# Optimization experiments

Hardware: AMD Instinct MI355X
Metric: run time of the kernel (lower is better)

Reference implementation:

```python
import jax, jax.numpy as jnp
import numpy as np
from jax import lax

CLASSES = 6
R = 8            # zoom_factor
FEAT = 32        # DUC loops i,j in range(32)
OUT_PAD = 304    # DUC hardcodes zeros(b,6,304,304)
IMG = 256        # original image H=W -> final bilinear resize target
BN_EPS = 1e-5
DN = ('NCHW', 'OIHW', 'NCHW')


def _duc(x):
    # x: [B, classes*r*r, H', W'] ; original loop only reads top-left 32x32
    x = x[:, :, :FEAT, :FEAT]
    B = x.shape[0]
    # channel order in original: view(b, classes, r*r) -> (classes, r, r)
    y = x.reshape(B, CLASSES, R, R, FEAT, FEAT)
    y = y.transpose(0, 1, 4, 2, 5, 3).reshape(B, CLASSES, FEAT * R, FEAT * R)  # [B,6,256,256]
    pad = OUT_PAD - FEAT * R
    return jnp.pad(y, ((0, 0), (0, 0), (0, pad), (0, pad)))  # zeros ring like torch.zeros buffer


def _bilinear_align_corners(x, oh, ow):
    b, c, h, w = x.shape
    ys = jnp.linspace(0.0, h - 1.0, oh)
    xs = jnp.linspace(0.0, w - 1.0, ow)
    y0 = jnp.floor(ys).astype(jnp.int32)
    x0 = jnp.floor(xs).astype(jnp.int32)
    y1 = jnp.minimum(y0 + 1, h - 1)
    x1 = jnp.minimum(x0 + 1, w - 1)
    wy = (ys - y0)[None, None, :, None]
    wx = (xs - x0)[None, None, None, :]
    rows = x[:, :, y0, :] * (1.0 - wy) + x[:, :, y1, :] * wy          # [b,c,oh,w]
    out = rows[:, :, :, x0] * (1.0 - wx) + rows[:, :, :, x1] * wx     # [b,c,oh,ow]
    return out


def setup_inputs() -> dict:
    key = jax.random.key(0)
    ks = jax.random.split(key, 8)
    x = jax.random.normal(ks[0], (16, 5632, 32, 32), jnp.float32)
    w1 = jax.random.normal(ks[1], (512, 5632, 1, 1), jnp.float32) * 0.02
    gamma = 1.0 + 0.1 * jax.random.normal(ks[2], (512,), jnp.float32)
    beta = 0.1 * jax.random.normal(ks[3], (512,), jnp.float32)
    mean = 0.1 * jax.random.normal(ks[4], (512,), jnp.float32)
    var = jax.random.uniform(ks[5], (512,), jnp.float32, 0.5, 1.5)
    w2 = jax.random.normal(ks[6], (CLASSES * R * R, 512, 1, 1), jnp.float32) * 0.02
    b2 = jax.random.normal(ks[7], (CLASSES * R * R,), jnp.float32) * 0.02
    return {'x': x, 'w1': w1, 'gamma': gamma, 'beta': beta, 'mean': mean, 'var': var, 'w2': w2, 'b2': b2}


def reference(x, w1, gamma, beta, mean, var, w2, b2):
    # cls head: 1x1 conv with padding=1 (quirk in source) -> 34x34 map
    h = lax.conv_general_dilated(x, w1, (1, 1), ((1, 1), (1, 1)), dimension_numbers=DN)
    inv = lax.rsqrt(var + BN_EPS)
    h = (h - mean[None, :, None, None]) * (inv * gamma)[None, :, None, None] + beta[None, :, None, None]
    h = jax.nn.relu(h)  # Dropout2d is identity at inference
    h = lax.conv_general_dilated(h, w2, (1, 1), ((0, 0), (0, 0)), dimension_numbers=DN)
    h = h + b2[None, :, None, None]            # [B,384,34,34]
    h = _duc(h)                                # [B,6,304,304]
    h = jax.nn.softmax(h, axis=1)
    return _bilinear_align_corners(h, IMG, IMG)  # [B,6,256,256]
```

## Files before the change

### kernel.cpp

```cpp
#include <hip/hip_runtime.h>
#include <hip/hip_bf16.h>
#include <stdint.h>

typedef float f32x4 __attribute__((ext_vector_type(4)));
typedef short s16x8 __attribute__((ext_vector_type(8)));
typedef unsigned short u16;

__device__ __forceinline__ u16 f2bf(float f) {
  uint32_t u = __float_as_uint(f);
  u = (u + 0x7fffu + ((u >> 16) & 1u)) >> 16;
  return (u16)u;
}

__global__ void k_params(const float* __restrict__ gamma, const float* __restrict__ beta,
                         const float* __restrict__ mean, const float* __restrict__ var,
                         float* __restrict__ bnS, float* __restrict__ bnT) {
  int i = threadIdx.x;
  if (i < 512) {
    float s = gamma[i] * rsqrtf(var[i] + 1e-5f);
    bnS[i] = s;
    bnT[i] = beta[i] - mean[i] * s;
  }
}

__global__ void k_convert(const float* __restrict__ in, u16* __restrict__ out, int n4) {
  int i = blockIdx.x * blockDim.x + threadIdx.x;
  if (i < n4) {
    float4 v = ((const float4*)in)[i];
    ushort4 o;
    o.x = f2bf(v.x); o.y = f2bf(v.y); o.z = f2bf(v.z); o.w = f2bf(v.w);
    ((ushort4*)out)[i] = o;
  }
}

__global__ void k_border2(const float* __restrict__ w2, const float* __restrict__ b2,
                          const float* __restrict__ bnT, float* __restrict__ border2) {
  int o = blockIdx.x;
  int l = threadIdx.x;
  float s = 0.f;
  for (int j = 0; j < 8; ++j) {
    int c = l + 64 * j;
    s += w2[o * 512 + c] * fmaxf(bnT[c], 0.f);
  }
  for (int off = 32; off > 0; off >>= 1) s += __shfl_down(s, off, 64);
  if (l == 0) border2[o] = s + b2[o];
}

__global__ __launch_bounds__(256) void k_trans(const float* __restrict__ x, u16* __restrict__ xT,
                                               int b0, int CB) {
  int id = blockIdx.x;
  int bl = id / (88 * 16);
  int rem = id - bl * 88 * 16;
  int ktile = rem >> 4;
  int ptile = rem & 15;
  __shared__ __align__(16) u16 tile[64 * 80];
  int t = threadIdx.x;
  int kl = t >> 2;
  int pb = (t & 3) * 16;
  const float* src = x + ((size_t)(b0 + bl) * 5632 + (size_t)(ktile * 64 + kl)) * 1024
                       + ptile * 64 + pb;
#pragma unroll
  for (int j = 0; j < 4; ++j) {
    float4 v = *(const float4*)(src + j * 4);
    int p = pb + j * 4;
    tile[(p + 0) * 80 + kl] = f2bf(v.x);
    tile[(p + 1) * 80 + kl] = f2bf(v.y);
    tile[(p + 2) * 80 + kl] = f2bf(v.z);
    tile[(p + 3) * 80 + kl] = f2bf(v.w);
  }
  __syncthreads();
#pragma unroll
  for (int j = 0; j < 2; ++j) {
    int q = t + j * 256;
    int pl = q >> 3, g = q & 7;
    s16x8 v = *(const s16x8*)(tile + pl * 80 + g * 8);
    *(s16x8*)(xT + (size_t)(bl * 1024 + ptile * 64 + pl) * 5632 + ktile * 64 + g * 8) = v;
  }
}

template <int MODE>
__global__ __launch_bounds__(256, 2) void k_gemm(
    const u16* __restrict__ A, const u16* __restrict__ B,
    int strideA, int strideB, int K, int nTN,
    const float* __restrict__ P0, const float* __restrict__ P1,
    void* __restrict__ Cout, int m_off) {
  __shared__ __align__(16) u16 sA[4096];
  __shared__ __align__(16) u16 sB[4096];
  int nb = gridDim.x;
  int id = blockIdx.x;
  int li = (id & 7) * (nb >> 3) + (id >> 3);
  int nt = li % nTN;
  int mt = li / nTN;
  int t = threadIdx.x;
  int l = t & 63, w = t >> 6;
  int wm = w >> 1, wn = w & 1;

  auto swz = [](int u) { int m = u >> 2, g = u & 3; return (m * 4 + (g ^ ((m >> 1) & 3))) * 8; };
  int wo0 = swz(t), wo1 = swz(t + 256);

  const u16* gA0 = A + (size_t)(mt * 128 + (t >> 2)) * strideA + (t & 3) * 8;
  const u16* gA1 = gA0 + (size_t)64 * strideA;
  const u16* gB0 = B + (size_t)(nt * 128 + (t >> 2)) * strideB + (t & 3) * 8;
  const u16* gB1 = gB0 + (size_t)64 * strideB;

  int offA[4], offB[4];
#pragma unroll
  for (int f = 0; f < 4; ++f) {
    int g = l >> 4;
    int m = wm * 64 + f * 16 + (l & 15);
    offA[f] = (m * 4 + (g ^ ((m >> 1) & 3))) * 8;
    int n = wn * 64 + f * 16 + (l & 15);
    offB[f] = (n * 4 + (g ^ ((n >> 1) & 3))) * 8;
  }

  f32x4 acc[4][4] = {};

  s16x8 rA0 = *(const s16x8*)gA0;
  s16x8 rA1 = *(const s16x8*)gA1;
  s16x8 rB0 = *(const s16x8*)gB0;
  s16x8 rB1 = *(const s16x8*)gB1;

  for (int k0 = 0; k0 < K; k0 += 32) {
    *(s16x8*)(sA + wo0) = rA0;
    *(s16x8*)(sA + wo1) = rA1;
    *(s16x8*)(sB + wo0) = rB0;
    *(s16x8*)(sB + wo1) = rB1;
    __syncthreads();
    if (k0 + 32 < K) {
      gA0 += 32; gA1 += 32; gB0 += 32; gB1 += 32;
      rA0 = *(const s16x8*)gA0;
      rA1 = *(const s16x8*)gA1;
      rB0 = *(const s16x8*)gB0;
      rB1 = *(const s16x8*)gB1;
    }
    s16x8 af[4], bf[4];
#pragma unroll
    for (int f = 0; f < 4; ++f) {
      af[f] = *(const s16x8*)(sA + offA[f]);
      bf[f] = *(const s16x8*)(sB + offB[f]);
    }
#pragma unroll
    for (int i = 0; i < 4; ++i)
#pragma unroll
      for (int j = 0; j < 4; ++j)
        acc[i][j] = __builtin_amdgcn_mfma_f32_16x16x32_bf16(af[i], bf[j], acc[i][j], 0, 0, 0);
    __syncthreads();
  }

  int mb = m_off + mt * 128 + wm * 64;
  int nbase = nt * 128 + wn * 64;
  if (MODE == 0) {
    u16* H = (u16*)Cout;
#pragma unroll
    for (int j = 0; j < 4; ++j) {
      int n_g = nbase + j * 16 + (l & 15);
      float s = P0[n_g], tt = P1[n_g];
#pragma unroll
      for (int i = 0; i < 4; ++i)
#pragma unroll
        for (int r = 0; r < 4; ++r) {
          int m_g = mb + i * 16 + (l >> 4) * 4 + r;
          float v = fmaxf(acc[i][j][r] * s + tt, 0.f);
          H[(size_t)m_g * 512 + n_g] = f2bf(v);
        }
    }
  } else {
    float* C = (float*)Cout;
#pragma unroll
    for (int j = 0; j < 4; ++j) {
      int n_g = nbase + j * 16 + (l & 15);
      float bias = P0[n_g];
#pragma unroll
      for (int i = 0; i < 4; ++i)
#pragma unroll
        for (int r = 0; r < 4; ++r) {
          int m_g = mb + i * 16 + (l >> 4) * 4 + r;
          C[(size_t)m_g * 384 + n_g] = acc[i][j][r] + bias;
        }
    }
  }
}

__global__ __launch_bounds__(256) void k_out(const float* __restrict__ c2,
                                             const float* __restrict__ border2,
                                             float* __restrict__ out) {
  int b = blockIdx.x >> 8;
  int oy = blockIdx.x & 255;
  int ox = threadIdx.x;
  const float SCL = 303.0f / 255.0f;
  float ys = oy * SCL, xs = ox * SCL;
  int y0 = (int)ys; if (y0 > 303) y0 = 303;
  int x0 = (int)xs; if (x0 > 303) x0 = 303;
  float wy = ys - (float)y0, wx = xs - (float)x0;
  int y1 = y0 + 1; if (y1 > 303) y1 = 303;
  int x1 = x0 + 1; if (x1 > 303) x1 = 303;
  int syA[2] = {y0, y1};
  int sxA[2] = {x0, x1};
  float wyA[2] = {1.f - wy, wy};
  float wxA[2] = {1.f - wx, wx};
  float acc[6] = {0.f, 0.f, 0.f, 0.f, 0.f, 0.f};
#pragma unroll
  for (int cy = 0; cy < 2; ++cy) {
#pragma unroll
    for (int cx = 0; cx < 2; ++cx) {
      float wgt = wyA[cy] * wxA[cx];
      int sy = syA[cy], sx = sxA[cx];
      if (sy >= 256 || sx >= 256) {
        float p = wgt * (1.f / 6.f);
#pragma unroll
        for (int c = 0; c < 6; ++c) acc[c] += p;
      } else {
        int i = sy >> 3, j = sx >> 3;
        int sub = ((sy & 7) << 3) | (sx & 7);
        const float* src;
        if (i == 0 || j == 0)
          src = border2 + sub;
        else
          src = c2 + (size_t)((b << 10) + ((i - 1) << 5) + (j - 1)) * 384 + sub;
        float l0 = src[0],   l1 = src[64],  l2 = src[128];
        float l3 = src[192], l4 = src[256], l5 = src[320];
        float mx = fmaxf(fmaxf(fmaxf(l0, l1), fmaxf(l2, l3)), fmaxf(l4, l5));
        float e0 = __expf(l0 - mx), e1 = __expf(l1 - mx), e2 = __expf(l2 - mx);
        float e3 = __expf(l3 - mx), e4 = __expf(l4 - mx), e5 = __expf(l5 - mx);
        float ssum = e0 + e1 + e2 + e3 + e4 + e5;
        float r = wgt / ssum;
        acc[0] += e0 * r; acc[1] += e1 * r; acc[2] += e2 * r;
        acc[3] += e3 * r; acc[4] += e4 * r; acc[5] += e5 * r;
      }
    }
  }
  size_t base = ((size_t)b * 6) << 16;
  int pix = (oy << 8) | ox;
#pragma unroll
  for (int c = 0; c < 6; ++c) out[base + ((size_t)c << 16) + pix] = acc[c];
}

extern "C" void kernel_launch(void* const* d_in, const int* in_sizes, int n_in,
                              void* d_out, int out_size, void* d_ws, size_t ws_size,
                              hipStream_t stream) {
  const float* x     = (const float*)d_in[0];
  const float* w1    = (const float*)d_in[1];
  const float* gamma = (const float*)d_in[2];
  const float* beta  = (const float*)d_in[3];
  const float* mean  = (const float*)d_in[4];
  const float* var   = (const float*)d_in[5];
  const float* w2    = (const float*)d_in[6];
  const float* b2    = (const float*)d_in[7];
  float* out = (float*)d_out;

  char* ws = (char*)d_ws;
  size_t off = 0;
  auto alloc = [&](size_t bytes) -> char* {
    char* p = ws + off;
    off = (off + bytes + 255) & ~(size_t)255;
    return p;
  };
  u16*   w1bf    = (u16*)alloc(512ull * 5632 * 2);
  u16*   w2bf    = (u16*)alloc(384ull * 512 * 2);
  float* bnS     = (float*)alloc(512 * 4);
  float* bnT     = (float*)alloc(512 * 4);
  float* border2 = (float*)alloc(384 * 4);
  u16*   h       = (u16*)alloc(16384ull * 512 * 2);
  float* c2      = (float*)alloc(16384ull * 384 * 4);

  const size_t xT_full = 16384ull * 5632 * 2;
  int nc = 1;
  while (nc < 16 && off + xT_full / nc + 4096 > ws_size) nc <<= 1;
  int CB = 16 / nc;
  u16* xT = (u16*)alloc(xT_full / nc);

  k_params<<<dim3(1), dim3(512), 0, stream>>>(gamma, beta, mean, var, bnS, bnT);
  k_convert<<<dim3(2816), dim3(256), 0, stream>>>(w1, w1bf, 512 * 5632 / 4);
  k_convert<<<dim3(192), dim3(256), 0, stream>>>(w2, w2bf, 384 * 512 / 4);
  k_border2<<<dim3(384), dim3(64), 0, stream>>>(w2, b2, bnT, border2);

  for (int c = 0; c < nc; ++c) {
    k_trans<<<dim3(CB * 88 * 16), dim3(256), 0, stream>>>(x, xT, c * CB, CB);
    k_gemm<0><<<dim3(CB * 8 * 4), dim3(256), 0, stream>>>(
        xT, w1bf, 5632, 5632, 5632, 4, bnS, bnT, (void*)h, c * CB * 1024);
  }
  k_gemm<1><<<dim3(128 * 3), dim3(256), 0, stream>>>(
      h, w2bf, 512, 512, 512, 3, b2, nullptr, (void*)c2, 0);
  k_out<<<dim3(16 * 256), dim3(256), 0, stream>>>(c2, border2, out);
}
```

Baseline: 302.4 us.

## Fuse fp32-to-bf16 transpose of x into first GEMM's A-tile load

Removes the separate transpose/convert kernel that wrote a bf16 K-major copy of x to workspace. The first GEMM now reads fp32 x directly with strided float2 loads along K, converts to bf16 in registers and stores into a padded LDS tile. This avoids writing and re-reading about 185MB of intermediate data, at the cost of less coalesced global loads (8 rows of 1024 stride per thread) and more conversion work inside the GEMM loop.

```diff
diff --git a/kernel.cpp b/kernel.cpp
--- a/kernel.cpp
+++ b/kernel.cpp
@@ -46,51 +46,117 @@
   if (l == 0) border2[o] = s + b2[o];
 }
 
-__global__ __launch_bounds__(256) void k_trans(const float* __restrict__ x, u16* __restrict__ xT,
-                                               int b0, int CB) {
+__global__ __launch_bounds__(256, 2) void k_gemm1(
+    const float* __restrict__ X, const u16* __restrict__ B,
+    const float* __restrict__ bnS, const float* __restrict__ bnT,
+    u16* __restrict__ H) {
+  const int K = 5632;
+  __shared__ __align__(16) u16 sA[128 * 40];
+  __shared__ __align__(16) u16 sB[4096];
+  int nb = gridDim.x;
   int id = blockIdx.x;
-  int bl = id / (88 * 16);
-  int rem = id - bl * 88 * 16;
-  int ktile = rem >> 4;
-  int ptile = rem & 15;
-  __shared__ __align__(16) u16 tile[64 * 80];
+  int li = (id & 7) * (nb >> 3) + (id >> 3);
+  int nt = li & 3;
+  int mt = li >> 2;
   int t = threadIdx.x;
-  int kl = t >> 2;
-  int pb = (t & 3) * 16;
-  const float* src = x + ((size_t)(b0 + bl) * 5632 + (size_t)(ktile * 64 + kl)) * 1024
-                       + ptile * 64 + pb;
+  int l = t & 63, w = t >> 6;
+  int wm = w >> 1, wn = w & 1;
+
+  auto swz = [](int u) { int m = u >> 2, g = u & 3; return (m * 4 + (g ^ ((m >> 1) & 3))) * 8; };
+  int wo0 = swz(t), wo1 = swz(t + 256);
+
+  int m0 = (w >> 1) * 64 + 2 * (l & 31);
+  int kh = w & 1;
+  int kq = l >> 5;
+  int bidx = mt >> 3, p0 = (mt & 7) * 128;
+  const float* gA = X + (size_t)bidx * (5632ull * 1024) + (size_t)(kh * 16 + kq * 8) * 1024
+                      + p0 + m0;
+  int aoff = m0 * 40 + kh * 16 + kq * 8;
+
+  const u16* gB0 = B + (size_t)(nt * 128 + (t >> 2)) * K + (t & 3) * 8;
+  const u16* gB1 = gB0 + (size_t)64 * K;
+
+  int offA[4], offB[4];
+#pragma unroll
+  for (int f = 0; f < 4; ++f) {
+    int m = wm * 64 + f * 16 + (l & 15);
+    offA[f] = m * 40 + (l >> 4) * 8;
+    int n = wn * 64 + f * 16 + (l & 15);
+    int g = l >> 4;
+    offB[f] = (n * 4 + (g ^ ((n >> 1) & 3))) * 8;
+  }
+
+  f32x4 acc[4][4] = {};
+
+  float2 va[8];
+  s16x8 rB0, rB1;
+#pragma unroll
+  for (int i = 0; i < 8; ++i) va[i] = *(const float2*)(gA + (size_t)i * 1024);
+  rB0 = *(const s16x8*)gB0;
+  rB1 = *(const s16x8*)gB1;
+
+  for (int k0 = 0; k0 < K; k0 += 32) {
+    union { u16 u[16]; s16x8 v[2]; } cv;
+#pragma unroll
+    for (int i = 0; i < 8; ++i) {
+      cv.u[i] = f2bf(va[i].x);
+      cv.u[8 + i] = f2bf(va[i].y);
+    }
+    *(s16x8*)(sA + aoff) = cv.v[0];
+    *(s16x8*)(sA + aoff + 40) = cv.v[1];
+    *(s16x8*)(sB + wo0) = rB0;
+    *(s16x8*)(sB + wo1) = rB1;
+    __syncthreads();
+    if (k0 + 32 < K) {
+      gA += 32 * 1024;
+      gB0 += 32; gB1 += 32;
+#pragma unroll
+      for (int i = 0; i < 8; ++i) va[i] = *(const float2*)(gA + (size_t)i * 1024);
+      rB0 = *(const s16x8*)gB0;
+      rB1 = *(const s16x8*)gB1;
+    }
+    s16x8 af[4], bf[4];
+#pragma unroll
+    for (int f = 0; f < 4; ++f) {
+      af[f] = *(const s16x8*)(sA + offA[f]);
+      bf[f] = *(const s16x8*)(sB + offB[f]);
+    }
+#pragma unroll
+    for (int i = 0; i < 4; ++i)
+#pragma unroll
+      for (int j = 0; j < 4; ++j)
+        acc[i][j] = __builtin_amdgcn_mfma_f32_16x16x32_bf16(af[i], bf[j], acc[i][j], 0, 0, 0);
+    __syncthreads();
+  }
+
+  int mb = mt * 128 + wm * 64;
+  int nbase = nt * 128 + wn * 64;
 #pragma unroll
   for (int j = 0; j < 4; ++j) {
-    float4 v = *(const float4*)(src + j * 4);
-    int p = pb + j * 4;
-    tile[(p + 0) * 80 + kl] = f2bf(v.x);
-    tile[(p + 1) * 80 + kl] = f2bf(v.y);
-    tile[(p + 2) * 80 + kl] = f2bf(v.z);
-    tile[(p + 3) * 80 + kl] = f2bf(v.w);
-  }
-  __syncthreads();
-#pragma unroll
-  for (int j = 0; j < 2; ++j) {
-    int q = t + j * 256;
-    int pl = q >> 3, g = q & 7;
-    s16x8 v = *(const s16x8*)(tile + pl * 80 + g * 8);
-    *(s16x8*)(xT + (size_t)(bl * 1024 + ptile * 64 + pl) * 5632 + ktile * 64 + g * 8) = v;
-  }
-}
-
-template <int MODE>
-__global__ __launch_bounds__(256, 2) void k_gemm(
+    int n_g = nbase + j * 16 + (l & 15);
+    float s = bnS[n_g], tt = bnT[n_g];
+#pragma unroll
+    for (int i = 0; i < 4; ++i)
+#pragma unroll
+      for (int r = 0; r < 4; ++r) {
+        int m_g = mb + i * 16 + (l >> 4) * 4 + r;
+        float v = fmaxf(acc[i][j][r] * s + tt, 0.f);
+        H[(size_t)m_g * 512 + n_g] = f2bf(v);
+      }
+  }
+}
+
+__global__ __launch_bounds__(256, 2) void k_gemm2(
     const u16* __restrict__ A, const u16* __restrict__ B,
-    int strideA, int strideB, int K, int nTN,
-    const float* __restrict__ P0, const float* __restrict__ P1,
-    void* __restrict__ Cout, int m_off) {
+    const float* __restrict__ b2, float* __restrict__ C) {
+  const int K = 512;
   __shared__ __align__(16) u16 sA[4096];
   __shared__ __align__(16) u16 sB[4096];
   int nb = gridDim.x;
   int id = blockIdx.x;
   int li = (id & 7) * (nb >> 3) + (id >> 3);
-  int nt = li % nTN;
-  int mt = li / nTN;
+  int nt = li % 3;
+  int mt = li / 3;
   int t = threadIdx.x;
   int l = t & 63, w = t >> 6;
   int wm = w >> 1, wn = w & 1;
@@ -98,10 +164,10 @@
   auto swz = [](int u) { int m = u >> 2, g = u & 3; return (m * 4 + (g ^ ((m >> 1) & 3))) * 8; };
   int wo0 = swz(t), wo1 = swz(t + 256);
 
-  const u16* gA0 = A + (size_t)(mt * 128 + (t >> 2)) * strideA + (t & 3) * 8;
-  const u16* gA1 = gA0 + (size_t)64 * strideA;
-  const u16* gB0 = B + (size_t)(nt * 128 + (t >> 2)) * strideB + (t & 3) * 8;
-  const u16* gB1 = gB0 + (size_t)64 * strideB;
+  const u16* gA0 = A + (size_t)(mt * 128 + (t >> 2)) * K + (t & 3) * 8;
+  const u16* gA1 = gA0 + (size_t)64 * K;
+  const u16* gB0 = B + (size_t)(nt * 128 + (t >> 2)) * K + (t & 3) * 8;
+  const u16* gB1 = gB0 + (size_t)64 * K;
 
   int offA[4], offB[4];
 #pragma unroll
@@ -147,37 +213,19 @@
     __syncthreads();
   }
 
-  int mb = m_off + mt * 128 + wm * 64;
+  int mb = mt * 128 + wm * 64;
   int nbase = nt * 128 + wn * 64;
-  if (MODE == 0) {
-    u16* H = (u16*)Cout;
-#pragma unroll
-    for (int j = 0; j < 4; ++j) {
-      int n_g = nbase + j * 16 + (l & 15);
-      float s = P0[n_g], tt = P1[n_g];
-#pragma unroll
-      for (int i = 0; i < 4; ++i)
-#pragma unroll
-        for (int r = 0; r < 4; ++r) {
-          int m_g = mb + i * 16 + (l >> 4) * 4 + r;
-          float v = fmaxf(acc[i][j][r] * s + tt, 0.f);
-          H[(size_t)m_g * 512 + n_g] = f2bf(v);
-        }
-    }
-  } else {
-    float* C = (float*)Cout;
-#pragma unroll
-    for (int j = 0; j < 4; ++j) {
-      int n_g = nbase + j * 16 + (l & 15);
-      float bias = P0[n_g];
-#pragma unroll
-      for (int i = 0; i < 4; ++i)
-#pragma unroll
-        for (int r = 0; r < 4; ++r) {
-          int m_g = mb + i * 16 + (l >> 4) * 4 + r;
-          C[(size_t)m_g * 384 + n_g] = acc[i][j][r] + bias;
-        }
-    }
+#pragma unroll
+  for (int j = 0; j < 4; ++j) {
+    int n_g = nbase + j * 16 + (l & 15);
+    float bias = b2[n_g];
+#pragma unroll
+    for (int i = 0; i < 4; ++i)
+#pragma unroll
+      for (int r = 0; r < 4; ++r) {
+        int m_g = mb + i * 16 + (l >> 4) * 4 + r;
+        C[(size_t)m_g * 384 + n_g] = acc[i][j][r] + bias;
+      }
   }
 }
 
@@ -262,24 +310,14 @@
   float* border2 = (float*)alloc(384 * 4);
   u16*   h       = (u16*)alloc(16384ull * 512 * 2);
   float* c2      = (float*)alloc(16384ull * 384 * 4);
-
-  const size_t xT_full = 16384ull * 5632 * 2;
-  int nc = 1;
-  while (nc < 16 && off + xT_full / nc + 4096 > ws_size) nc <<= 1;
-  int CB = 16 / nc;
-  u16* xT = (u16*)alloc(xT_full / nc);
+  (void)ws_size;
 
   k_params<<<dim3(1), dim3(512), 0, stream>>>(gamma, beta, mean, var, bnS, bnT);
   k_convert<<<dim3(2816), dim3(256), 0, stream>>>(w1, w1bf, 512 * 5632 / 4);
   k_convert<<<dim3(192), dim3(256), 0, stream>>>(w2, w2bf, 384 * 512 / 4);
   k_border2<<<dim3(384), dim3(64), 0, stream>>>(w2, b2, bnT, border2);
 
-  for (int c = 0; c < nc; ++c) {
-    k_trans<<<dim3(CB * 88 * 16), dim3(256), 0, stream>>>(x, xT, c * CB, CB);
-    k_gemm<0><<<dim3(CB * 8 * 4), dim3(256), 0, stream>>>(
-        xT, w1bf, 5632, 5632, 5632, 4, bnS, bnT, (void*)h, c * CB * 1024);
-  }
-  k_gemm<1><<<dim3(128 * 3), dim3(256), 0, stream>>>(
-      h, w2bf, 512, 512, 512, 3, b2, nullptr, (void*)c2, 0);
+  k_gemm1<<<dim3(512), dim3(256), 0, stream>>>(x, w1bf, bnS, bnT, h);
+  k_gemm2<<<dim3(128 * 3), dim3(256), 0, stream>>>(h, w2bf, b2, c2);
   k_out<<<dim3(16 * 256), dim3(256), 0, stream>>>(c2, border2, out);
 }
```

Result: faster. 260.5 us (-13.9%).

## Split-K first GEMM with direct global-to-LDS loads and combine kernel

Applied to the files above, without the earlier changes.

Rewrites the large first 1x1-conv GEMM so that, when workspace allows, the K dimension is split in two. This doubles the grid to 1024 blocks for better CU occupancy, and the fp32 partials are reduced in a separate kernel that also applies BN, ReLU and the bf16 conversion. The GEMM main loop now loads tiles with global_load_lds directly into unswizzled LDS, replacing register staging, and drops the 2-blocks-per-CU launch bound. The cost is an extra 64MB fp32 partial write and read plus possible LDS bank conflicts and a loss of load/compute overlap from the single-buffered sync loop.

```diff
diff --git a/kernel.cpp b/kernel.cpp
--- a/kernel.cpp
+++ b/kernel.cpp
@@ -11,6 +11,17 @@
   u = (u + 0x7fffu + ((u >> 16) & 1u)) >> 16;
   return (u16)u;
 }
+
+__device__ __forceinline__ u16 cvt_bf(float f) {
+  union { __hip_bfloat16 h; u16 u; } c;
+  c.h = __float2bfloat16(f);
+  return c.u;
+}
+
+#define GLDS16(gsrc, ldst)                                                    \
+  __builtin_amdgcn_global_load_lds(                                           \
+      (const __attribute__((address_space(1))) void*)(gsrc),                  \
+      (__attribute__((address_space(3))) void*)(ldst), 16, 0, 0)
 
 __global__ void k_params(const float* __restrict__ gamma, const float* __restrict__ beta,
                          const float* __restrict__ mean, const float* __restrict__ var,
@@ -79,18 +90,124 @@
 }
 
 template <int MODE>
-__global__ __launch_bounds__(256, 2) void k_gemm(
+__global__ __launch_bounds__(256) void k_gemm1t(
+    const u16* __restrict__ A, const u16* __restrict__ Bw,
+    const float* __restrict__ bnS, const float* __restrict__ bnT,
+    u16* __restrict__ H, float* __restrict__ P, int m_off, int nMT) {
+  const int K = 5632;
+  const int KS = (MODE == 1) ? 2816 : 5632;
+  __shared__ __align__(16) u16 sA[4096];
+  __shared__ __align__(16) u16 sB[4096];
+  int id = blockIdx.x;
+  int nInner = nMT * 4;
+  int inner = (MODE == 1) ? (id % nInner) : id;
+  int kh = (MODE == 1) ? (id / nInner) : 0;
+  int kbase = kh * 2816;
+  int li = (inner % 8) * (nInner / 8) + inner / 8;
+  int nt = li & 3;
+  int mt = li >> 2;
+  int t = threadIdx.x;
+  int l = t & 63, w = t >> 6;
+  int wm = w >> 1, wn = w & 1;
+
+  const u16* gA = A + (size_t)(mt * 128 + (t >> 2)) * K + kbase + (t & 3) * 8;
+  const u16* gB = Bw + (size_t)(nt * 128 + (t >> 2)) * K + kbase + (t & 3) * 8;
+  const size_t rstep = (size_t)64 * K;
+  char* dA0 = (char*)sA + w * 1024;
+  char* dA1 = (char*)sA + 4096 + w * 1024;
+  char* dB0 = (char*)sB + w * 1024;
+  char* dB1 = (char*)sB + 4096 + w * 1024;
+
+  int offA[4], offB[4];
+#pragma unroll
+  for (int f = 0; f < 4; ++f) {
+    offA[f] = (wm * 64 + f * 16 + (l & 15)) * 64 + (l >> 4) * 16;
+    offB[f] = (wn * 64 + f * 16 + (l & 15)) * 64 + (l >> 4) * 16;
+  }
+
+  f32x4 acc[4][4] = {};
+
+  for (int k0 = 0; k0 < KS; k0 += 32) {
+    GLDS16(gA, dA0);
+    GLDS16(gA + rstep, dA1);
+    GLDS16(gB, dB0);
+    GLDS16(gB + rstep, dB1);
+    gA += 32; gB += 32;
+    __syncthreads();
+    s16x8 af[4], bf[4];
+#pragma unroll
+    for (int f = 0; f < 4; ++f) {
+      af[f] = *(const s16x8*)((const char*)sA + offA[f]);
+      bf[f] = *(const s16x8*)((const char*)sB + offB[f]);
+    }
+#pragma unroll
+    for (int i = 0; i < 4; ++i)
+#pragma unroll
+      for (int j = 0; j < 4; ++j)
+        acc[i][j] = __builtin_amdgcn_mfma_f32_16x16x32_bf16(af[i], bf[j], acc[i][j], 0, 0, 0);
+    __syncthreads();
+  }
+
+  int mb = m_off + mt * 128 + wm * 64;
+  int nbase = nt * 128 + wn * 64;
+  if (MODE == 0) {
+#pragma unroll
+    for (int j = 0; j < 4; ++j) {
+      int n_g = nbase + j * 16 + (l & 15);
+      float s = bnS[n_g], tt = bnT[n_g];
+#pragma unroll
+      for (int i = 0; i < 4; ++i)
+#pragma unroll
+        for (int r = 0; r < 4; ++r) {
+          int m_g = mb + i * 16 + (l >> 4) * 4 + r;
+          float v = fmaxf(acc[i][j][r] * s + tt, 0.f);
+          H[(size_t)m_g * 512 + n_g] = f2bf(v);
+        }
+    }
+  } else {
+    float* Pd = P + (size_t)kh * (16384ull * 512);
+#pragma unroll
+    for (int j = 0; j < 4; ++j) {
+      int n_g = nbase + j * 16 + (l & 15);
+#pragma unroll
+      for (int i = 0; i < 4; ++i)
+#pragma unroll
+        for (int r = 0; r < 4; ++r) {
+          int m_g = mb + i * 16 + (l >> 4) * 4 + r;
+          Pd[(size_t)m_g * 512 + n_g] = acc[i][j][r];
+        }
+    }
+  }
+}
+
+__global__ __launch_bounds__(256) void k_combine(
+    const float* __restrict__ P, const float* __restrict__ bnS,
+    const float* __restrict__ bnT, u16* __restrict__ H) {
+  int i = blockIdx.x * 256 + threadIdx.x;
+  const float4 a = ((const float4*)P)[i];
+  const float4 b = ((const float4*)(P + 16384ull * 512))[i];
+  int n0 = (i * 4) & 511;
+  float4 s = *(const float4*)(bnS + n0);
+  float4 tt = *(const float4*)(bnT + n0);
+  ushort4 o;
+  o.x = cvt_bf(fmaxf((a.x + b.x) * s.x + tt.x, 0.f));
+  o.y = cvt_bf(fmaxf((a.y + b.y) * s.y + tt.y, 0.f));
+  o.z = cvt_bf(fmaxf((a.z + b.z) * s.z + tt.z, 0.f));
+  o.w = cvt_bf(fmaxf((a.w + b.w) * s.w + tt.w, 0.f));
+  ((ushort4*)H)[i] = o;
+}
+
+__global__ __launch_bounds__(256, 2) void k_gemm2(
     const u16* __restrict__ A, const u16* __restrict__ B,
-    int strideA, int strideB, int K, int nTN,
-    const float* __restrict__ P0, const float* __restrict__ P1,
-    void* __restrict__ Cout, int m_off) {
+    const float* __restrict__ b2, float* __restrict__ C) {
+  const int K = 512;
   __shared__ __align__(16) u16 sA[4096];
   __shared__ __align__(16) u16 sB[4096];
   int nb = gridDim.x;
   int id = blockIdx.x;
   int li = (id & 7) * (nb >> 3) + (id >> 3);
-  int nt = li % nTN;
-  int mt = li / nTN;
+  int nt = li % 3;
+  int mt = li / 3;
   int t = threadIdx.x;
   int l = t & 63, w = t >> 6;
   int wm = w >> 1, wn = w & 1;
@@ -98,10 +215,10 @@
   auto swz = [](int u) { int m = u >> 2, g = u & 3; return (m * 4 + (g ^ ((m >> 1) & 3))) * 8; };
   int wo0 = swz(t), wo1 = swz(t + 256);
 
-  const u16* gA0 = A + (size_t)(mt * 128 + (t >> 2)) * strideA + (t & 3) * 8;
-  const u16* gA1 = gA0 + (size_t)64 * strideA;
-  const u16* gB0 = B + (size_t)(nt * 128 + (t >> 2)) * strideB + (t & 3) * 8;
-  const u16* gB1 = gB0 + (size_t)64 * strideB;
+  const u16* gA0 = A + (size_t)(mt * 128 + (t >> 2)) * K + (t & 3) * 8;
+  const u16* gA1 = gA0 + (size_t)64 * K;
+  const u16* gB0 = B + (size_t)(nt * 128 + (t >> 2)) * K + (t & 3) * 8;
+  const u16* gB1 = gB0 + (size_t)64 * K;
 
   int offA[4], offB[4];
 #pragma unroll
@@ -147,37 +264,19 @@
     __syncthreads();
   }
 
-  int mb = m_off + mt * 128 + wm * 64;
+  int mb = mt * 128 + wm * 64;
   int nbase = nt * 128 + wn * 64;
-  if (MODE == 0) {
-    u16* H = (u16*)Cout;
-#pragma unroll
-    for (int j = 0; j < 4; ++j) {
-      int n_g = nbase + j * 16 + (l & 15);
-      float s = P0[n_g], tt = P1[n_g];
-#pragma unroll
-      for (int i = 0; i < 4; ++i)
-#pragma unroll
-        for (int r = 0; r < 4; ++r) {
-          int m_g = mb + i * 16 + (l >> 4) * 4 + r;
-          float v = fmaxf(acc[i][j][r] * s + tt, 0.f);
-          H[(size_t)m_g * 512 + n_g] = f2bf(v);
-        }
-    }
-  } else {
-    float* C = (float*)Cout;
-#pragma unroll
-    for (int j = 0; j < 4; ++j) {
-      int n_g = nbase + j * 16 + (l & 15);
-      float bias = P0[n_g];
-#pragma unroll
-      for (int i = 0; i < 4; ++i)
-#pragma unroll
-        for (int r = 0; r < 4; ++r) {
-          int m_g = mb + i * 16 + (l >> 4) * 4 + r;
-          C[(size_t)m_g * 384 + n_g] = acc[i][j][r] + bias;
-        }
-    }
+#pragma unroll
+  for (int j = 0; j < 4; ++j) {
+    int n_g = nbase + j * 16 + (l & 15);
+    float bias = b2[n_g];
+#pragma unroll
+    for (int i = 0; i < 4; ++i)
+#pragma unroll
+      for (int r = 0; r < 4; ++r) {
+        int m_g = mb + i * 16 + (l >> 4) * 4 + r;
+        C[(size_t)m_g * 384 + n_g] = acc[i][j][r] + bias;
+      }
   }
 }
 
@@ -263,23 +362,35 @@
   u16*   h       = (u16*)alloc(16384ull * 512 * 2);
   float* c2      = (float*)alloc(16384ull * 384 * 4);
 
-  const size_t xT_full = 16384ull * 5632 * 2;
-  int nc = 1;
-  while (nc < 16 && off + xT_full / nc + 4096 > ws_size) nc <<= 1;
-  int CB = 16 / nc;
-  u16* xT = (u16*)alloc(xT_full / nc);
+  const size_t XT  = 16384ull * 5632 * 2;
+  const size_t PB2 = 2 * 16384ull * 512 * 4;
 
   k_params<<<dim3(1), dim3(512), 0, stream>>>(gamma, beta, mean, var, bnS, bnT);
   k_convert<<<dim3(2816), dim3(256), 0, stream>>>(w1, w1bf, 512 * 5632 / 4);
   k_convert<<<dim3(192), dim3(256), 0, stream>>>(w2, w2bf, 384 * 512 / 4);
   k_border2<<<dim3(384), dim3(64), 0, stream>>>(w2, b2, bnT, border2);
 
-  for (int c = 0; c < nc; ++c) {
-    k_trans<<<dim3(CB * 88 * 16), dim3(256), 0, stream>>>(x, xT, c * CB, CB);
-    k_gemm<0><<<dim3(CB * 8 * 4), dim3(256), 0, stream>>>(
-        xT, w1bf, 5632, 5632, 5632, 4, bnS, bnT, (void*)h, c * CB * 1024);
-  }
-  k_gemm<1><<<dim3(128 * 3), dim3(256), 0, stream>>>(
-      h, w2bf, 512, 512, 512, 3, b2, nullptr, (void*)c2, 0);
+  if (off + XT + PB2 + 4096 <= ws_size) {
+    u16*   xT = (u16*)alloc(XT);
+    float* P  = (float*)alloc(PB2);
+    k_trans<<<dim3(16 * 88 * 16), dim3(256), 0, stream>>>(x, xT, 0, 16);
+    k_gemm1t<1><<<dim3(1024), dim3(256), 0, stream>>>(xT, w1bf, bnS, bnT, h, P, 0, 128);
+    k_combine<<<dim3(8192), dim3(256), 0, stream>>>(P, bnS, bnT, h);
+  } else if (off + XT + 4096 <= ws_size) {
+    u16* xT = (u16*)alloc(XT);
+    k_trans<<<dim3(16 * 88 * 16), dim3(256), 0, stream>>>(x, xT, 0, 16);
+    k_gemm1t<0><<<dim3(512), dim3(256), 0, stream>>>(xT, w1bf, bnS, bnT, h, nullptr, 0, 128);
+  } else {
+    int nc = 2;
+    while (nc < 16 && off + XT / nc + 4096 > ws_size) nc <<= 1;
+    int CB = 16 / nc;
+    u16* xT = (u16*)alloc(XT / nc);
+    for (int c = 0; c < nc; ++c) {
+      k_trans<<<dim3(CB * 88 * 16), dim3(256), 0, stream>>>(x, xT, c * CB, CB);
+      k_gemm1t<0><<<dim3(CB * 8 * 4), dim3(256), 0, stream>>>(
+          xT, w1bf, bnS, bnT, h, nullptr, c * CB * 1024, CB * 8);
+    }
+  }
+  k_gemm2<<<dim3(128 * 3), dim3(256), 0, stream>>>(h, w2bf, b2, c2);
   k_out<<<dim3(16 * 256), dim3(256), 0, stream>>>(c2, border2, out);
 }
```

Measured after the change: 349.0 us. 15.4% more time.
